# Optimization experiments

Measured on AMD Instinct MI355X. Metric: run time of the kernel, lower is better.

Reference implementation:

```python
import jax, jax.numpy as jnp
import numpy as np

B = 64
E = 512          # latent_size / h_dim
H = 8            # num_heads
D = E // H       # head_dim
MAX_AGENTS = 254 # max(agents_per_sample) for the deterministic counts below
NEG = -1e9


def setup_inputs() -> dict:
    key = jax.random.key(0)
    k_x, k_wi, k_bi, k_wo, k_bo = jax.random.split(key, 5)
    # deterministic variable agent counts in [128, 254]; sum == 11531, max == 254
    agents = jnp.array([128 + (3 * i) % 129 for i in range(B)], dtype=jnp.int32)
    total = 11531
    att_in = jax.random.normal(k_x, (total, E), dtype=jnp.float32)
    # nn.MultiheadAttention params: packed in-proj [3E, E] + bias, out-proj [E, E] + bias
    w_in = jax.random.normal(k_wi, (3 * E, E), dtype=jnp.float32) * 0.02
    b_in = jax.random.normal(k_bi, (3 * E,), dtype=jnp.float32) * 0.02
    w_out = jax.random.normal(k_wo, (E, E), dtype=jnp.float32) * 0.02
    b_out = jax.random.normal(k_bo, (E,), dtype=jnp.float32) * 0.02
    return {"att_in": att_in, "w_in": w_in, "b_in": b_in,
            "w_out": w_out, "b_out": b_out, "agents_per_sample": agents}


def reference(att_in, w_in, b_in, w_out, b_out, agents_per_sample):
    S = MAX_AGENTS
    # scatter packed rows into padded [B, S, E] via a clipped gather (jit-safe)
    offsets = jnp.cumsum(agents_per_sample) - agents_per_sample      # [B]
    pos = jnp.arange(S, dtype=jnp.int32)
    mask = pos[None, :] < agents_per_sample[:, None]                 # [B, S] valid
    idx = jnp.clip(offsets[:, None] + pos[None, :], 0, att_in.shape[0] - 1)
    padded = jnp.where(mask[..., None], att_in[idx], 0.0)            # [B, S, E]

    # fused QKV projection (torch packed in_proj), dropout disabled (eval)
    qkv = padded @ w_in.T + b_in                                     # [B, S, 3E]
    q, k, v = jnp.split(qkv, 3, axis=-1)
    q = q.reshape(B, S, H, D)
    k = k.reshape(B, S, H, D)
    v = v.reshape(B, S, H, D)

    scores = jnp.einsum('bqhd,bkhd->bhqk', q, k) * (D ** -0.5)      # [B, H, S, S]
    scores = jnp.where(mask[:, None, None, :], scores, NEG)          # key_padding_mask
    attn = jax.nn.softmax(scores, axis=-1)
    ctx = jnp.einsum('bhqk,bkhd->bqhd', attn, v).reshape(B, S, E)
    out = ctx @ w_out.T + b_out                                      # [B, S, E]
    # torch returns only valid rows per sample; zero the padded rows instead
    return out * mask[..., None]
```

## Files before the change

kernel.cpp:

```cpp
#include <hip/hip_runtime.h>
#include <hip/hip_bf16.h>

typedef __attribute__((ext_vector_type(8))) short bf16x8;
typedef __attribute__((ext_vector_type(4))) float f32x4;
typedef __attribute__((ext_vector_type(4))) int i32x4;
typedef __attribute__((ext_vector_type(4))) unsigned short u16x4;
typedef __attribute__((ext_vector_type(2))) unsigned ui2;
typedef __attribute__((ext_vector_type(4))) float fl4;

struct __attribute__((packed)) u16x4u { u16x4 v; };

__device__ __forceinline__ f32x4 mfma16(bf16x8 a, bf16x8 b, f32x4 c) {
    return __builtin_amdgcn_mfma_f32_16x16x32_bf16(a, b, c, 0, 0, 0);
}

__device__ __forceinline__ unsigned short f2b(float f) {
    unsigned u = __float_as_uint(f);
    unsigned r = (u + 0x7FFF + ((u >> 16) & 1)) >> 16;
    return (unsigned short)r;
}

__device__ __forceinline__ int bsearch_off(const int* s_off, int m) {
    int lo = 0, hi = 63;
    while (lo < hi) {
        int mid = (lo + hi + 1) >> 1;
        if (s_off[mid] <= m) lo = mid; else hi = mid - 1;
    }
    return lo;
}

__device__ __forceinline__ void gld_lds16(const __hip_bfloat16* g, __hip_bfloat16* l) {
    __builtin_amdgcn_global_load_lds(
        (const __attribute__((address_space(1))) void*)g,
        (__attribute__((address_space(3))) void*)l,
        16, 0, 0);
}

__global__ void k_prep(const unsigned short* __restrict__ src,
                       const void* __restrict__ b_in, const void* __restrict__ b_out,
                       const int* __restrict__ agents,
                       int* __restrict__ flag, int* __restrict__ offs,
                       float* __restrict__ bfi, float* __restrict__ bfo) {
    __shared__ int sh[256];
    __shared__ int sa[64];
    __shared__ int sflag;
    int tid = threadIdx.x;
    int h = 0;
    for (int i = tid; i < 16384; i += 256) {
        unsigned e = (src[i] >> 7) & 0xFF;
        if (e == 0xFF) h = 1;
    }
    sh[tid] = h;
    if (tid < 64) sa[tid] = agents[tid];
    __syncthreads();
    if (tid == 0) {
        int any = 0;
        for (int i = 0; i < 256; ++i) any |= sh[i];
        flag[0] = any;
        sflag = any;
    }
    if (tid < 64) {
        int ex = 0;
        for (int i = 0; i < 64; ++i) { int v = sa[i]; if (i < tid) ex += v; }
        offs[tid] = ex;
        if (tid == 63) offs[64] = ex + sa[63];
    }
    __syncthreads();
    int f = sflag;
    for (int i = tid; i < 1536; i += 256)
        bfi[i] = f ? ((const float*)b_in)[i]
                   : __bfloat162float(((const __hip_bfloat16*)b_in)[i]);
    for (int i = tid; i < 512; i += 256)
        bfo[i] = f ? ((const float*)b_out)[i]
                   : __bfloat162float(((const __hip_bfloat16*)b_out)[i]);
}

__global__ void k_zero(char* __restrict__ out, long long out_elems, const int* __restrict__ flag) {
    long long bytes = flag[0] ? out_elems * 4 : out_elems * 2;
    long long i = ((long long)blockIdx.x * 256 + threadIdx.x) * 16;
    if (i < bytes) *(i32x4*)(out + i) = (i32x4){0, 0, 0, 0};
}

__global__ void k_cast(const void* __restrict__ src, unsigned short* __restrict__ dst,
                       int n, const int* __restrict__ flag) {
    int i = (blockIdx.x * 256 + threadIdx.x) * 4;
    if (i >= n) return;
    u16x4 o;
    if (flag[0]) {
        fl4 v = *(const fl4*)((const float*)src + i);
        o[0] = f2b(v[0]); o[1] = f2b(v[1]); o[2] = f2b(v[2]); o[3] = f2b(v[3]);
    } else {
        o = *(const u16x4*)((const unsigned short*)src + i);
    }
    *(u16x4*)(dst + i) = o;
}

template<int LDA, bool MROWS>
__device__ __forceinline__ void gemm_core(
    const __hip_bfloat16* __restrict__ A,
    const __hip_bfloat16* __restrict__ W,
    int m0, int n0, int total,
    __hip_bfloat16* As, __hip_bfloat16* Ws,
    f32x4 acc[4][4], int tid)
{
    int lane = tid & 63, quad = lane >> 4, c = lane & 15;
    int wave = tid >> 6;
    int wr = wave >> 1, wc = wave & 1;

    int chunk0 = tid;
    int chunk1 = 256 + tid;
    int ar0 = m0 + (chunk0 >> 2); if (ar0 > total - 1) ar0 = total - 1;
    int ar1 = m0 + (chunk1 >> 2); if (ar1 > total - 1) ar1 = total - 1;
    const __hip_bfloat16* gA0 = A + (size_t)ar0 * LDA + (chunk0 & 3) * 8;
    const __hip_bfloat16* gA1 = A + (size_t)ar1 * LDA + (chunk1 & 3) * 8;
    const __hip_bfloat16* gW0 = W + (size_t)(n0 + (chunk0 >> 2)) * 512 + (chunk0 & 3) * 8;
    const __hip_bfloat16* gW1 = W + (size_t)(n0 + (chunk1 >> 2)) * 512 + (chunk1 & 3) * 8;
    __hip_bfloat16* lA0 = As + (size_t)(wave * 64) * 8;
    __hip_bfloat16* lA1 = As + (size_t)(256 + wave * 64) * 8;
    __hip_bfloat16* lW0 = Ws + (size_t)(wave * 64) * 8;
    __hip_bfloat16* lW1 = Ws + (size_t)(256 + wave * 64) * 8;

    for (int k0 = 0; k0 < 512; k0 += 32) {
        if (k0) __syncthreads();
        gld_lds16(gA0 + k0, lA0);
        gld_lds16(gA1 + k0, lA1);
        gld_lds16(gW0 + k0, lW0);
        gld_lds16(gW1 + k0, lW1);
        __syncthreads();
        bf16x8 af[4], wf[4];
#pragma unroll
        for (int t = 0; t < 4; ++t) {
            af[t] = *(const bf16x8*)(As + (size_t)(wr * 64 + t * 16 + c) * 32 + quad * 8);
            wf[t] = *(const bf16x8*)(Ws + (size_t)(wc * 64 + t * 16 + c) * 32 + quad * 8);
        }
#pragma unroll
        for (int i = 0; i < 4; ++i)
#pragma unroll
            for (int j = 0; j < 4; ++j)
                acc[i][j] = MROWS ? mfma16(af[i], wf[j], acc[i][j])
                                  : mfma16(wf[j], af[i], acc[i][j]);
    }
}

__global__ __launch_bounds__(256) void k_qkv(
    const __hip_bfloat16* __restrict__ A,
    const __hip_bfloat16* __restrict__ W,
    const float* __restrict__ bias,
    const int* __restrict__ offs,
    __hip_bfloat16* __restrict__ qk,
    __hip_bfloat16* __restrict__ vT,
    int total, int MT)
{
    __shared__ __hip_bfloat16 As[128 * 32];
    __shared__ __hip_bfloat16 Ws[128 * 32];
    __shared__ int s_off[65];
    int l = blockIdx.x;
    int inner = l >> 3;
    int cb = inner % 12;
    int rb = (l & 7) + 8 * (inner / 12);
    if (rb >= MT) return;
    int n0 = cb * 128;
    int m0 = rb * 128;
    int tid = threadIdx.x;
    if (tid < 65) s_off[tid] = offs[tid];
    int lane = tid & 63, quad = lane >> 4, c = lane & 15;
    int wave = tid >> 6, wr = wave >> 1, wc = wave & 1;
    f32x4 z = {0.f, 0.f, 0.f, 0.f};
    f32x4 acc[4][4] = {{z,z,z,z},{z,z,z,z},{z,z,z,z},{z,z,z,z}};

    if (n0 < 1024) {
        gemm_core<512, false>(A, W, m0, n0, total, As, Ws, acc, tid);
        fl4 bv4[4];
#pragma unroll
        for (int j = 0; j < 4; ++j)
            bv4[j] = *(const fl4*)&bias[n0 + wc * 64 + j * 16 + quad * 4];
#pragma unroll
        for (int i = 0; i < 4; ++i) {
            int m = m0 + wr * 64 + i * 16 + c;
            if (m >= total) continue;
            size_t row = (size_t)m * 1024;
#pragma unroll
            for (int j = 0; j < 4; ++j) {
                int col0 = n0 + wc * 64 + j * 16 + quad * 4;
                u16x4 o;
#pragma unroll
                for (int r = 0; r < 4; ++r) o[r] = f2b(acc[i][j][r] + bv4[j][r]);
                *(u16x4*)&qk[row + col0] = o;
            }
        }
    } else {
        gemm_core<512, true>(A, W, m0, n0, total, As, Ws, acc, tid);
        float bv[4];
#pragma unroll
        for (int j = 0; j < 4; ++j) bv[j] = bias[n0 + wc * 64 + j * 16 + c];
#pragma unroll
        for (int i = 0; i < 4; ++i) {
            int m_base = m0 + wr * 64 + i * 16 + quad * 4;
            if (m_base >= total) continue;
            int lo = bsearch_off(s_off, m_base);
            bool vec = (m_base + 3 < total) && (s_off[lo + 1] > m_base + 3);
            if (vec) {
                int vs = m_base - s_off[lo];
#pragma unroll
                for (int j = 0; j < 4; ++j) {
                    int vc = n0 - 1024 + wc * 64 + j * 16 + c;
                    size_t idx = ((size_t)(lo * 8 + (vc >> 6)) * 64 + (vc & 63)) * 256 + vs;
                    u16x4 o;
#pragma unroll
                    for (int r = 0; r < 4; ++r) o[r] = f2b(acc[i][j][r] + bv[j]);
                    ((u16x4u*)&vT[idx])->v = o;
                }
            } else {
#pragma unroll
                for (int r = 0; r < 4; ++r) {
                    int m = m_base + r;
                    if (m >= total) continue;
                    int lo2 = bsearch_off(s_off, m);
                    int vs2 = m - s_off[lo2];
#pragma unroll
                    for (int j = 0; j < 4; ++j) {
                        int vc = n0 - 1024 + wc * 64 + j * 16 + c;
                        vT[((size_t)(lo2 * 8 + (vc >> 6)) * 64 + (vc & 63)) * 256 + vs2] =
                            __float2bfloat16(acc[i][j][r] + bv[j]);
                    }
                }
            }
        }
    }
}

__global__ __launch_bounds__(256, 2) void k_attn(
    __hip_bfloat16* __restrict__ qk,
    const __hip_bfloat16* __restrict__ vT,
    const int* __restrict__ agents,
    const int* __restrict__ offs)
{
    __shared__ __attribute__((aligned(16))) char Pl[4][16 * 80];
    int bh = blockIdx.x;
    int b = bh >> 3, h = bh & 7;
    int n = agents[b];
    int off = offs[b];
    int qtiles = (n + 15) >> 4;
    int stmax = (qtiles + 1) >> 1;
    int tid = threadIdx.x;
    int wave = tid >> 6, lane = tid & 63, quad = lane >> 4, c = lane & 15;
    const __hip_bfloat16* vbase = vT + (size_t)bh * 64 * 256;
    char* Plw = &Pl[wave][0];

    bf16x8 qB[4][2];
    int nt = 0;
#pragma unroll
    for (int t = 0; t < 4; ++t) {
        int qt = wave + 4 * t;
        if (qt < qtiles) {
            nt = t + 1;
            int qr = qt * 16 + c; if (qr > n - 1) qr = n - 1;
            const __hip_bfloat16* qp = qk + (size_t)(off + qr) * 1024 + h * 64 + quad * 8;
            qB[t][0] = *(const bf16x8*)qp;
            qB[t][1] = *(const bf16x8*)(qp + 32);
        }
    }

    f32x4 z = {0.f, 0.f, 0.f, 0.f};
    f32x4 O[4][4] = {{z,z,z,z},{z,z,z,z},{z,z,z,z},{z,z,z,z}};
    float sm[4] = {0.f, 0.f, 0.f, 0.f};
    const __hip_bfloat16* kg = qk + (size_t)off * 1024 + 512 + h * 64 + quad * 8;

    for (int st = 0; st < stmax; ++st) {
        int k0 = st * 32;
        bf16x8 kA[2][2];
#pragma unroll
        for (int ti = 0; ti < 2; ++ti) {
            int kr = k0 + ti * 16 + c; if (kr > n - 1) kr = n - 1;
            const __hip_bfloat16* kp = kg + (size_t)kr * 1024;
            kA[ti][0] = *(const bf16x8*)kp;
            kA[ti][1] = *(const bf16x8*)(kp + 32);
        }
        bf16x8 vA[4];
#pragma unroll
        for (int dt = 0; dt < 4; ++dt)
            vA[dt] = *(const bf16x8*)(vbase + (size_t)(dt * 16 + c) * 256 + k0 + quad * 8);

#pragma unroll
        for (int t = 0; t < 4; ++t) {
            if (t < nt) {
#pragma unroll
                for (int ti = 0; ti < 2; ++ti) {
                    f32x4 s = mfma16(kA[ti][0], qB[t][0], z);
                    s = mfma16(kA[ti][1], qB[t][1], s);
                    int kbase = k0 + ti * 16 + quad * 4;
                    float p0 = (kbase + 0 < n) ? __expf(s[0] * 0.125f) : 0.f;
                    float p1 = (kbase + 1 < n) ? __expf(s[1] * 0.125f) : 0.f;
                    float p2 = (kbase + 2 < n) ? __expf(s[2] * 0.125f) : 0.f;
                    float p3 = (kbase + 3 < n) ? __expf(s[3] * 0.125f) : 0.f;
                    sm[t] += (p0 + p1) + (p2 + p3);
                    ui2 dw;
                    dw[0] = (unsigned)f2b(p0) | ((unsigned)f2b(p1) << 16);
                    dw[1] = (unsigned)f2b(p2) | ((unsigned)f2b(p3) << 16);
                    *(ui2*)(Plw + c * 80 + ti * 32 + quad * 8) = dw;
                }
                bf16x8 pB = *(const bf16x8*)(Plw + c * 80 + quad * 16);
#pragma unroll
                for (int dt = 0; dt < 4; ++dt)
                    O[t][dt] = mfma16(vA[dt], pB, O[t][dt]);
            }
        }
    }

#pragma unroll
    for (int t = 0; t < 4; ++t) {
        if (t < nt) {
            float v = sm[t];
            v += __shfl_xor(v, 16);
            v += __shfl_xor(v, 32);
            float iv = 1.0f / v;
            int q = (wave + 4 * t) * 16 + c;
            if (q < n) {
                size_t row = (size_t)(off + q) * 1024 + h * 64;
#pragma unroll
                for (int dt = 0; dt < 4; ++dt) {
                    u16x4 o;
#pragma unroll
                    for (int r = 0; r < 4; ++r) o[r] = f2b(O[t][dt][r] * iv);
                    *(u16x4*)&qk[row + dt * 16 + quad * 4] = o;
                }
            }
        }
    }
}

__global__ __launch_bounds__(256) void k_out(
    const __hip_bfloat16* __restrict__ A,
    const __hip_bfloat16* __restrict__ W,
    const float* __restrict__ bias,
    const int* __restrict__ offs,
    void* __restrict__ out,
    const int* __restrict__ flag,
    int total, int MT)
{
    __shared__ __hip_bfloat16 As[128 * 32];
    __shared__ __hip_bfloat16 Ws[128 * 32];
    __shared__ int s_off[65];
    int l = blockIdx.x;
    int inner = l >> 3;
    int cb = inner & 3;
    int rb = (l & 7) + 8 * (inner >> 2);
    if (rb >= MT) return;
    int n0 = cb * 128;
    int m0 = rb * 128;
    int tid = threadIdx.x;
    if (tid < 65) s_off[tid] = offs[tid];
    f32x4 z = {0.f, 0.f, 0.f, 0.f};
    f32x4 acc[4][4] = {{z,z,z,z},{z,z,z,z},{z,z,z,z},{z,z,z,z}};
    gemm_core<1024, false>(A, W, m0, n0, total, As, Ws, acc, tid);

    int f32m = flag[0];
    int lane = tid & 63, quad = lane >> 4, c = lane & 15;
    int wave = tid >> 6, wr = wave >> 1, wc = wave & 1;
    fl4 bv4[4];
#pragma unroll
    for (int j = 0; j < 4; ++j)
        bv4[j] = *(const fl4*)&bias[n0 + wc * 64 + j * 16 + quad * 4];
#pragma unroll
    for (int i = 0; i < 4; ++i) {
        int m = m0 + wr * 64 + i * 16 + c;
        if (m >= total) continue;
        int lo = bsearch_off(s_off, m);
        int os_ = m - s_off[lo];
        size_t rowb = ((size_t)(lo * 254 + os_)) * 512;
#pragma unroll
        for (int j = 0; j < 4; ++j) {
            int col0 = n0 + wc * 64 + j * 16 + quad * 4;
            if (f32m) {
                fl4 o;
#pragma unroll
                for (int r = 0; r < 4; ++r) o[r] = acc[i][j][r] + bv4[j][r];
                *(fl4*)&((float*)out)[rowb + col0] = o;
            } else {
                u16x4 o;
#pragma unroll
                for (int r = 0; r < 4; ++r) o[r] = f2b(acc[i][j][r] + bv4[j][r]);
                *(u16x4*)&((__hip_bfloat16*)out)[rowb + col0] = o;
            }
        }
    }
}

extern "C" void kernel_launch(void* const* d_in, const int* in_sizes, int n_in,
                              void* d_out, int out_size, void* d_ws, size_t ws_size,
                              hipStream_t stream) {
    const void* att_in = d_in[0];
    const void* w_in   = d_in[1];
    const void* b_in   = d_in[2];
    const void* w_out  = d_in[3];
    const void* b_out  = d_in[4];
    const int* agents  = (const int*)d_in[5];
    int total = in_sizes[0] / 512;

    char* p = (char*)d_ws;
    int* flag  = (int*)p;                 p += 256;
    int* offs  = (int*)p;                 p += 512;
    float* bfi = (float*)p;               p += 1536 * 4;
    float* bfo = (float*)p;               p += 512 * 4;
    __hip_bfloat16* WinBf  = (__hip_bfloat16*)p;  p += (size_t)1536 * 512 * 2;
    __hip_bfloat16* WoutBf = (__hip_bfloat16*)p;  p += (size_t)512 * 512 * 2;
    __hip_bfloat16* Abf    = (__hip_bfloat16*)p;  p += (size_t)total * 512 * 2;
    __hip_bfloat16* qk     = (__hip_bfloat16*)p;  p += (size_t)total * 1024 * 2;
    __hip_bfloat16* vT     = (__hip_bfloat16*)p;  p += (size_t)64 * 8 * 64 * 256 * 2;

    int nA = total * 512, nWi = 1536 * 512, nWo = 512 * 512;

    k_prep<<<1, 256, 0, stream>>>((const unsigned short*)att_in, b_in, b_out,
                                  agents, flag, offs, bfi, bfo);
    long long zblocks = ((long long)out_size * 4 / 16 + 255) / 256;
    k_zero<<<(int)zblocks, 256, 0, stream>>>((char*)d_out, out_size, flag);
    k_cast<<<(nA / 4 + 255) / 256, 256, 0, stream>>>(att_in, (unsigned short*)Abf, nA, flag);
    k_cast<<<(nWi / 4 + 255) / 256, 256, 0, stream>>>(w_in, (unsigned short*)WinBf, nWi, flag);
    k_cast<<<(nWo / 4 + 255) / 256, 256, 0, stream>>>(w_out, (unsigned short*)WoutBf, nWo, flag);

    int MT = (total + 127) / 128;
    int MTpad = ((MT + 7) / 8) * 8;
    k_qkv<<<12 * MTpad, 256, 0, stream>>>(Abf, WinBf, bfi, offs, qk, vT, total, MT);
    k_attn<<<512, 256, 0, stream>>>(qk, vT, agents, offs);
    k_out<<<4 * MTpad, 256, 0, stream>>>(qk, WoutBf, bfo, offs, d_out, flag, total, MT);
}
```

Measured before the change: 188.0 us.

## Deepen GEMM K-tile to 64 with XOR-swizzled LDS, merge cast kernels, zero only padding

The shared GEMM core now stages 64-wide K slices instead of 32, halving the number of barrier-separated load rounds. It applies an XOR swizzle on 16-byte segments so the fragment reads from LDS avoid bank conflicts. The three bf16 cast launches are merged into one kernel, and the output zeroing now writes only each sample's padded rows instead of the whole output. Costs are doubled LDS per block, which may lower occupancy, and the new cast kernel branches per thread on which buffer it handles.

```diff
diff --git a/kernel.cpp b/kernel.cpp
--- a/kernel.cpp
+++ b/kernel.cpp
@@ -75,24 +75,36 @@
                    : __bfloat162float(((const __hip_bfloat16*)b_out)[i]);
 }
 
-__global__ void k_zero(char* __restrict__ out, long long out_elems, const int* __restrict__ flag) {
-    long long bytes = flag[0] ? out_elems * 4 : out_elems * 2;
-    long long i = ((long long)blockIdx.x * 256 + threadIdx.x) * 16;
-    if (i < bytes) *(i32x4*)(out + i) = (i32x4){0, 0, 0, 0};
-}
-
-__global__ void k_cast(const void* __restrict__ src, unsigned short* __restrict__ dst,
-                       int n, const int* __restrict__ flag) {
+__global__ void k_zero_pad(char* __restrict__ out, const int* __restrict__ agents,
+                           const int* __restrict__ flag) {
+    int b = blockIdx.x;
+    int n = agents[b];
+    int esz = flag[0] ? 4 : 2;
+    long long base = ((long long)b * 254 + n) * 512 * esz;
+    long long bytes = (long long)(254 - n) * 512 * esz;
+    for (long long i = ((long long)blockIdx.y * 256 + threadIdx.x) * 16;
+         i < bytes; i += (long long)8 * 256 * 16)
+        *(i32x4*)(out + base + i) = (i32x4){0, 0, 0, 0};
+}
+
+__global__ void k_cast_all(const void* __restrict__ sA, unsigned short* __restrict__ dA, int nA,
+                           const void* __restrict__ sWi, unsigned short* __restrict__ dWi, int nWi,
+                           const void* __restrict__ sWo, unsigned short* __restrict__ dWo, int nWo,
+                           const int* __restrict__ flag) {
     int i = (blockIdx.x * 256 + threadIdx.x) * 4;
-    if (i >= n) return;
+    const void* src; unsigned short* dst; int k;
+    if (i < nA)            { src = sA;  dst = dA;  k = i; }
+    else if (i < nA + nWi) { src = sWi; dst = dWi; k = i - nA; }
+    else if (i < nA + nWi + nWo) { src = sWo; dst = dWo; k = i - nA - nWi; }
+    else return;
     u16x4 o;
     if (flag[0]) {
-        fl4 v = *(const fl4*)((const float*)src + i);
+        fl4 v = *(const fl4*)((const float*)src + k);
         o[0] = f2b(v[0]); o[1] = f2b(v[1]); o[2] = f2b(v[2]); o[3] = f2b(v[3]);
     } else {
-        o = *(const u16x4*)((const unsigned short*)src + i);
-    }
-    *(u16x4*)(dst + i) = o;
+        o = *(const u16x4*)((const unsigned short*)src + k);
+    }
+    *(u16x4*)(dst + k) = o;
 }
 
 template<int LDA, bool MROWS>
@@ -107,38 +119,47 @@
     int wave = tid >> 6;
     int wr = wave >> 1, wc = wave & 1;
 
-    int chunk0 = tid;
-    int chunk1 = 256 + tid;
-    int ar0 = m0 + (chunk0 >> 2); if (ar0 > total - 1) ar0 = total - 1;
-    int ar1 = m0 + (chunk1 >> 2); if (ar1 > total - 1) ar1 = total - 1;
-    const __hip_bfloat16* gA0 = A + (size_t)ar0 * LDA + (chunk0 & 3) * 8;
-    const __hip_bfloat16* gA1 = A + (size_t)ar1 * LDA + (chunk1 & 3) * 8;
-    const __hip_bfloat16* gW0 = W + (size_t)(n0 + (chunk0 >> 2)) * 512 + (chunk0 & 3) * 8;
-    const __hip_bfloat16* gW1 = W + (size_t)(n0 + (chunk1 >> 2)) * 512 + (chunk1 & 3) * 8;
-    __hip_bfloat16* lA0 = As + (size_t)(wave * 64) * 8;
-    __hip_bfloat16* lA1 = As + (size_t)(256 + wave * 64) * 8;
-    __hip_bfloat16* lW0 = Ws + (size_t)(wave * 64) * 8;
-    __hip_bfloat16* lW1 = Ws + (size_t)(256 + wave * 64) * 8;
-
-    for (int k0 = 0; k0 < 512; k0 += 32) {
+    const __hip_bfloat16* gA[4];
+    const __hip_bfloat16* gW[4];
+    __hip_bfloat16* lA[4];
+    __hip_bfloat16* lW[4];
+#pragma unroll
+    for (int j = 0; j < 4; ++j) {
+        int L = j * 256 + tid;
+        int row = L >> 3;
+        int gseg = (L & 7) ^ (row & 7);
+        int ar = m0 + row; if (ar > total - 1) ar = total - 1;
+        gA[j] = A + (size_t)ar * LDA + gseg * 8;
+        gW[j] = W + (size_t)(n0 + row) * 512 + gseg * 8;
+        lA[j] = As + (size_t)(j * 256 + wave * 64) * 8;
+        lW[j] = Ws + (size_t)(j * 256 + wave * 64) * 8;
+    }
+
+    for (int k0 = 0; k0 < 512; k0 += 64) {
         if (k0) __syncthreads();
-        gld_lds16(gA0 + k0, lA0);
-        gld_lds16(gA1 + k0, lA1);
-        gld_lds16(gW0 + k0, lW0);
-        gld_lds16(gW1 + k0, lW1);
+#pragma unroll
+        for (int j = 0; j < 4; ++j) gld_lds16(gA[j] + k0, lA[j]);
+#pragma unroll
+        for (int j = 0; j < 4; ++j) gld_lds16(gW[j] + k0, lW[j]);
         __syncthreads();
-        bf16x8 af[4], wf[4];
-#pragma unroll
-        for (int t = 0; t < 4; ++t) {
-            af[t] = *(const bf16x8*)(As + (size_t)(wr * 64 + t * 16 + c) * 32 + quad * 8);
-            wf[t] = *(const bf16x8*)(Ws + (size_t)(wc * 64 + t * 16 + c) * 32 + quad * 8);
-        }
-#pragma unroll
-        for (int i = 0; i < 4; ++i)
-#pragma unroll
-            for (int j = 0; j < 4; ++j)
-                acc[i][j] = MROWS ? mfma16(af[i], wf[j], acc[i][j])
-                                  : mfma16(wf[j], af[i], acc[i][j]);
+#pragma unroll
+        for (int h = 0; h < 2; ++h) {
+            bf16x8 af[4], wf[4];
+#pragma unroll
+            for (int t = 0; t < 4; ++t) {
+                int rowa = wr * 64 + t * 16 + c;
+                int rowb = wc * 64 + t * 16 + c;
+                int ks = quad + 4 * h;
+                af[t] = *(const bf16x8*)(As + (size_t)rowa * 64 + ((ks ^ (rowa & 7)) * 8));
+                wf[t] = *(const bf16x8*)(Ws + (size_t)rowb * 64 + ((ks ^ (rowb & 7)) * 8));
+            }
+#pragma unroll
+            for (int i = 0; i < 4; ++i)
+#pragma unroll
+                for (int j = 0; j < 4; ++j)
+                    acc[i][j] = MROWS ? mfma16(af[i], wf[j], acc[i][j])
+                                      : mfma16(wf[j], af[i], acc[i][j]);
+        }
     }
 }
 
@@ -151,8 +172,8 @@
     __hip_bfloat16* __restrict__ vT,
     int total, int MT)
 {
-    __shared__ __hip_bfloat16 As[128 * 32];
-    __shared__ __hip_bfloat16 Ws[128 * 32];
+    __shared__ __hip_bfloat16 As[128 * 64];
+    __shared__ __hip_bfloat16 Ws[128 * 64];
     __shared__ int s_off[65];
     int l = blockIdx.x;
     int inner = l >> 3;
@@ -338,8 +359,8 @@
     const int* __restrict__ flag,
     int total, int MT)
 {
-    __shared__ __hip_bfloat16 As[128 * 32];
-    __shared__ __hip_bfloat16 Ws[128 * 32];
+    __shared__ __hip_bfloat16 As[128 * 64];
+    __shared__ __hip_bfloat16 Ws[128 * 64];
     __shared__ int s_off[65];
     int l = blockIdx.x;
     int inner = l >> 3;
@@ -409,14 +430,15 @@
     __hip_bfloat16* vT     = (__hip_bfloat16*)p;  p += (size_t)64 * 8 * 64 * 256 * 2;
 
     int nA = total * 512, nWi = 1536 * 512, nWo = 512 * 512;
+    int ntot = nA + nWi + nWo;
 
     k_prep<<<1, 256, 0, stream>>>((const unsigned short*)att_in, b_in, b_out,
                                   agents, flag, offs, bfi, bfo);
-    long long zblocks = ((long long)out_size * 4 / 16 + 255) / 256;
-    k_zero<<<(int)zblocks, 256, 0, stream>>>((char*)d_out, out_size, flag);
-    k_cast<<<(nA / 4 + 255) / 256, 256, 0, stream>>>(att_in, (unsigned short*)Abf, nA, flag);
-    k_cast<<<(nWi / 4 + 255) / 256, 256, 0, stream>>>(w_in, (unsigned short*)WinBf, nWi, flag);
-    k_cast<<<(nWo / 4 + 255) / 256, 256, 0, stream>>>(w_out, (unsigned short*)WoutBf, nWo, flag);
+    k_zero_pad<<<dim3(64, 8), 256, 0, stream>>>((char*)d_out, agents, flag);
+    k_cast_all<<<(ntot / 4 + 255) / 256, 256, 0, stream>>>(
+        att_in, (unsigned short*)Abf, nA,
+        w_in,   (unsigned short*)WinBf, nWi,
+        w_out,  (unsigned short*)WoutBf, nWo, flag);
 
     int MT = (total + 127) / 128;
     int MTpad = ((MT + 7) / 8) * 8;
```

Result: faster. 180.1 us (-4.2%).
